# Kernel tuning notes

Measured on AMD Instinct MI355X. Metric: run time of the kernel, lower is better.

## Reference

```python
import jax, jax.numpy as jnp
import numpy as np

N_NODES = 10000
N_EDGES = 320000
D_IN = 256
D_HID = 256
N_TASKS = 128
N_GRAPHS = 128


def gcn_conv(x, W, b, src, dst, inv_sqrt_deg, n_nodes):
    # PyG GCNConv: x' = W x, then symmetric-normalized scatter-add over
    # edges (self-loops already included in src/dst), plus bias.
    h = x @ W  # [N, D_out]
    norm = inv_sqrt_deg[src] * inv_sqrt_deg[dst]  # [E+N]
    msg = h[src] * norm[:, None]  # [E+N, D_out] gathered messages
    out = jax.ops.segment_sum(msg, dst, num_segments=n_nodes)
    return out + b


def setup_inputs() -> dict:
    key = jax.random.key(0)
    ks = jax.random.split(key, 10)
    x = jax.random.normal(ks[0], (N_NODES, D_IN), dtype=jnp.float32)
    edge_index = jax.random.randint(ks[1], (2, N_EDGES), 0, N_NODES, dtype=jnp.int64)
    batch = jnp.sort(jax.random.randint(ks[2], (N_NODES,), 0, N_GRAPHS, dtype=jnp.int64))
    s = 1.0 / np.sqrt(D_HID)
    W1 = jax.random.uniform(ks[3], (D_IN, D_HID), jnp.float32, -s, s)
    b1 = jnp.zeros((D_HID,), jnp.float32)
    W2 = jax.random.uniform(ks[4], (D_HID, D_HID), jnp.float32, -s, s)
    b2 = jnp.zeros((D_HID,), jnp.float32)
    W3 = jax.random.uniform(ks[5], (D_HID, D_HID), jnp.float32, -s, s)
    b3 = jnp.zeros((D_HID,), jnp.float32)
    lin_w = jax.random.uniform(ks[6], (D_HID, N_TASKS), jnp.float32, -s, s)
    lin_b = jax.random.uniform(ks[7], (N_TASKS,), jnp.float32, -s, s)
    return {"x": x, "edge_index": edge_index, "batch": batch,
            "W1": W1, "b1": b1, "W2": W2, "b2": b2, "W3": W3, "b3": b3,
            "lin_w": lin_w, "lin_b": lin_b}


def reference(x, edge_index, batch, W1, b1, W2, b2, W3, b3, lin_w, lin_b):
    n = x.shape[0]
    loops = jnp.arange(n, dtype=edge_index.dtype)
    src = jnp.concatenate([edge_index[0], loops])  # add self-loops
    dst = jnp.concatenate([edge_index[1], loops])
    deg = jax.ops.segment_sum(jnp.ones_like(dst, dtype=x.dtype), dst, num_segments=n)
    inv_sqrt_deg = jnp.where(deg > 0, jax.lax.rsqrt(jnp.maximum(deg, 1.0)), 0.0)

    h = jax.nn.relu(gcn_conv(x, W1, b1, src, dst, inv_sqrt_deg, n))
    h = jax.nn.relu(gcn_conv(h, W2, b2, src, dst, inv_sqrt_deg, n))
    h = jax.nn.relu(gcn_conv(h, W3, b3, src, dst, inv_sqrt_deg, n))

    # global_mean_pool over graph ids
    sums = jax.ops.segment_sum(h, batch, num_segments=N_GRAPHS)  # [G, D]
    counts = jax.ops.segment_sum(jnp.ones((n,), h.dtype), batch, num_segments=N_GRAPHS)
    pooled = sums / jnp.maximum(counts, 1.0)[:, None]
    return pooled @ lin_w + lin_b  # [G, num_tasks]
```

## Files before the change

kernel.cpp:

```cpp
#include <hip/hip_runtime.h>

#define N_NODES  10000
#define N_EDGES  320000
#define D        256
#define N_TASKS  128
#define N_GRAPHS 128

#define CSR_BLOCKS 256
#define EPB (N_EDGES / CSR_BLOCKS)

typedef __attribute__((ext_vector_type(8))) _Float16 half8;
typedef __attribute__((ext_vector_type(4))) float floatx4;

__device__ __forceinline__ unsigned short f2h(float f) {
    _Float16 h = (_Float16)f;
    return *(unsigned short*)&h;
}
__device__ __forceinline__ float h2f(unsigned short u) {
    _Float16 h = *(_Float16*)&u;
    return (float)h;
}


__global__ __launch_bounds__(256) void histp_kernel(const int* __restrict__ dst,
                                                    unsigned short* __restrict__ histbuf,
                                                    unsigned short* __restrict__ rank) {
    __shared__ int h[N_NODES];
    int b = blockIdx.x, t = threadIdx.x;
    for (int i = t; i < N_NODES; i += 256) h[i] = 0;
    __syncthreads();
    int e0 = b * EPB;
    for (int i = t; i < EPB; i += 256) {
        int e = e0 + i;
        int r = atomicAdd(&h[dst[e]], 1);
        rank[e] = (unsigned short)r;
    }
    __syncthreads();
    unsigned short* outp = histbuf + (size_t)b * N_NODES;
    for (int i = t; i < N_NODES; i += 256) outp[i] = (unsigned short)h[i];
}

__global__ __launch_bounds__(256) void merge_kernel(unsigned short* __restrict__ histbuf,
                                                    int* __restrict__ cnt) {
    int n = blockIdx.x * 256 + threadIdx.x;
    if (n >= N_NODES) return;
    int run = 0;
#pragma unroll 1
    for (int b = 0; b < CSR_BLOCKS; b += 8) {
        int v0 = histbuf[(size_t)(b + 0) * N_NODES + n];
        int v1 = histbuf[(size_t)(b + 1) * N_NODES + n];
        int v2 = histbuf[(size_t)(b + 2) * N_NODES + n];
        int v3 = histbuf[(size_t)(b + 3) * N_NODES + n];
        int v4 = histbuf[(size_t)(b + 4) * N_NODES + n];
        int v5 = histbuf[(size_t)(b + 5) * N_NODES + n];
        int v6 = histbuf[(size_t)(b + 6) * N_NODES + n];
        int v7 = histbuf[(size_t)(b + 7) * N_NODES + n];
        histbuf[(size_t)(b + 0) * N_NODES + n] = (unsigned short)run; run += v0;
        histbuf[(size_t)(b + 1) * N_NODES + n] = (unsigned short)run; run += v1;
        histbuf[(size_t)(b + 2) * N_NODES + n] = (unsigned short)run; run += v2;
        histbuf[(size_t)(b + 3) * N_NODES + n] = (unsigned short)run; run += v3;
        histbuf[(size_t)(b + 4) * N_NODES + n] = (unsigned short)run; run += v4;
        histbuf[(size_t)(b + 5) * N_NODES + n] = (unsigned short)run; run += v5;
        histbuf[(size_t)(b + 6) * N_NODES + n] = (unsigned short)run; run += v6;
        histbuf[(size_t)(b + 7) * N_NODES + n] = (unsigned short)run; run += v7;
    }
    cnt[n] = run + 1;
}

__global__ __launch_bounds__(256) void scan_kernel(const int* __restrict__ cnt,
                                                   int* __restrict__ rowptr,
                                                   float* __restrict__ isd) {
    __shared__ int scnt[10240];
    __shared__ int part[256];
    const int CH = 40;
    int t = threadIdx.x;
    for (int i = t; i < 2500; i += 256) ((int4*)scnt)[i] = ((const int4*)cnt)[i];
    for (int i = 10000 + t; i < 10240; i += 256) scnt[i] = 1;
    __syncthreads();
    int base = t * CH;
    int s = 0;
#pragma unroll 8
    for (int i = 0; i < CH; ++i) s += scnt[base + i] - 1;
    part[t] = s;
    __syncthreads();
    for (int off = 1; off < 256; off <<= 1) {
        int v = (t >= off) ? part[t - off] : 0;
        __syncthreads();
        part[t] += v;
        __syncthreads();
    }
    int run = (t == 0) ? 0 : part[t - 1];
    for (int i = 0; i < CH; ++i) {
        int idx = base + i;
        if (idx < N_NODES) {
            rowptr[idx] = run;
            int c = scnt[idx];
            run += c - 1;
            isd[idx] = rsqrtf((float)c);
        }
    }
    if (t == 255) rowptr[N_NODES] = run;
}

__global__ __launch_bounds__(256) void scatter_kernel(const int* __restrict__ src,
                                                      const int* __restrict__ dst,
                                                      const unsigned short* __restrict__ rank,
                                                      const int* __restrict__ rowptr,
                                                      const unsigned short* __restrict__ histbuf,
                                                      const float* __restrict__ isd,
                                                      int2* __restrict__ edat) {
    int e = blockIdx.x * 256 + threadIdx.x;
    if (e >= N_EDGES) return;
    int b = e / EPB;
    int s = src[e], d = dst[e];
    int pos = rowptr[d] + (int)histbuf[(size_t)b * N_NODES + d] + (int)rank[e];
    edat[pos] = make_int2(s, __float_as_int(isd[s] * isd[d]));
}

__global__ __launch_bounds__(256) void wsplit_kernel(const float* __restrict__ W1,
                                                     const float* __restrict__ W2,
                                                     const float* __restrict__ W3,
                                                     unsigned short* __restrict__ wt) {
    __shared__ float t[32][33];
    int b = blockIdx.x;
    int w = b >> 6, tile = b & 63;
    int kt = (tile >> 3) << 5, nt = (tile & 7) << 5;
    const float* W = (w == 0) ? W1 : (w == 1) ? W2 : W3;
    int tid = threadIdx.x, r = tid >> 5, c = tid & 31;
#pragma unroll
    for (int i = 0; i < 4; ++i)
        t[r + 8 * i][c] = W[(size_t)(kt + r + 8 * i) * D + nt + c];
    __syncthreads();
    unsigned short* oh = wt + w * D * D;
#pragma unroll
    for (int i = 0; i < 4; ++i)
        oh[(size_t)(nt + r + 8 * i) * D + kt + c] = f2h(t[c][r + 8 * i]);
}

template <int F32IN>
__global__ __launch_bounds__(256) void mm_kernel(const void* __restrict__ Av,
                                                 const unsigned short* __restrict__ Wt,
                                                 unsigned short* __restrict__ C) {
    __shared__ unsigned short sA[64][40], sW[64][40];
    int tid = threadIdx.x;
    int lane = tid & 63, wid = tid >> 6;
    int wr = wid >> 1, wc = wid & 1;
    int row0 = blockIdx.x << 6;
    int n0 = blockIdx.y << 6;

    int sr = tid >> 2;
    int sk = (tid & 3) << 3;
    int arow = row0 + sr; if (arow >= N_NODES) arow = N_NODES - 1;
    const float*          pAf = (const float*)Av + (size_t)arow * D + sk;
    const unsigned short* pAh = (const unsigned short*)Av + (size_t)arow * D + sk;
    const unsigned short* pW  = Wt + (size_t)(n0 + sr) * D + sk;

    float4 rf0, rf1; uint4 rAh;
    if (F32IN) { rf0 = *(const float4*)pAf; rf1 = *(const float4*)(pAf + 4); }
    else       { rAh = *(const uint4*)pAh; }
    uint4 rW = *(const uint4*)pW;

    int fr = lane & 15;
    int fk = (lane >> 4) << 3;

    floatx4 acc00 = {0.f, 0.f, 0.f, 0.f};
    floatx4 acc01 = acc00, acc10 = acc00, acc11 = acc00;

#pragma unroll 1
    for (int step = 0; step < D / 32; ++step) {
        if (F32IN) {
            float vv[8] = {rf0.x, rf0.y, rf0.z, rf0.w, rf1.x, rf1.y, rf1.z, rf1.w};
            union { unsigned short u[8]; uint4 v; } ph;
#pragma unroll
            for (int j = 0; j < 8; ++j) ph.u[j] = f2h(vv[j]);
            *(uint4*)&sA[sr][sk] = ph.v;
        } else {
            *(uint4*)&sA[sr][sk] = rAh;
        }
        *(uint4*)&sW[sr][sk] = rW;
        __syncthreads();
        if (step < D / 32 - 1) {
            if (F32IN) {
                rf0 = *(const float4*)(pAf + (step + 1) * 32);
                rf1 = *(const float4*)(pAf + (step + 1) * 32 + 4);
            } else {
                rAh = *(const uint4*)(pAh + (step + 1) * 32);
            }
            rW = *(const uint4*)(pW + (step + 1) * 32);
        }
        half8 a0 = *(const half8*)&sA[(wr << 5) + fr][fk];
        half8 a1 = *(const half8*)&sA[(wr << 5) + 16 + fr][fk];
        half8 b0 = *(const half8*)&sW[(wc << 5) + fr][fk];
        half8 b1 = *(const half8*)&sW[(wc << 5) + 16 + fr][fk];
        acc00 = __builtin_amdgcn_mfma_f32_16x16x32_f16(a0, b0, acc00, 0, 0, 0);
        acc01 = __builtin_amdgcn_mfma_f32_16x16x32_f16(a0, b1, acc01, 0, 0, 0);
        acc10 = __builtin_amdgcn_mfma_f32_16x16x32_f16(a1, b0, acc10, 0, 0, 0);
        acc11 = __builtin_amdgcn_mfma_f32_16x16x32_f16(a1, b1, acc11, 0, 0, 0);
        __syncthreads();
    }

    int crow = (lane >> 4) << 2;
    int colbase = n0 + (wc << 5) + fr;
#pragma unroll
    for (int r = 0; r < 4; ++r) {
        int gr0 = row0 + (wr << 5) + crow + r;
        if (gr0 < N_NODES) {
            C[(size_t)gr0 * D + colbase]      = f2h(acc00[r]);
            C[(size_t)gr0 * D + colbase + 16] = f2h(acc01[r]);
        }
        int gr1 = gr0 + 16;
        if (gr1 < N_NODES) {
            C[(size_t)gr1 * D + colbase]      = f2h(acc10[r]);
            C[(size_t)gr1 * D + colbase + 16] = f2h(acc11[r]);
        }
    }
}

__device__ __forceinline__ void fma8(uint4 q, float wt, float* acc) {
    acc[0] = fmaf(h2f((unsigned short)(q.x & 0xffff)), wt, acc[0]);
    acc[1] = fmaf(h2f((unsigned short)(q.x >> 16)),    wt, acc[1]);
    acc[2] = fmaf(h2f((unsigned short)(q.y & 0xffff)), wt, acc[2]);
    acc[3] = fmaf(h2f((unsigned short)(q.y >> 16)),    wt, acc[3]);
    acc[4] = fmaf(h2f((unsigned short)(q.z & 0xffff)), wt, acc[4]);
    acc[5] = fmaf(h2f((unsigned short)(q.z >> 16)),    wt, acc[5]);
    acc[6] = fmaf(h2f((unsigned short)(q.w & 0xffff)), wt, acc[6]);
    acc[7] = fmaf(h2f((unsigned short)(q.w >> 16)),    wt, acc[7]);
}

__global__ __launch_bounds__(256) void agg_kernel(const unsigned short* __restrict__ h,
                                                  const int* __restrict__ rowptr,
                                                  const int2* __restrict__ edat,
                                                  const float* __restrict__ isd,
                                                  const float* __restrict__ bias,
                                                  unsigned short* __restrict__ outh) {
    int node = (blockIdx.x * blockDim.x + threadIdx.x) >> 6;
    if (node >= N_NODES) return;
    int lane = threadIdx.x & 63;
    int half = lane >> 5;
    int sub  = lane & 31;

    float acc[8] = {0.f, 0.f, 0.f, 0.f, 0.f, 0.f, 0.f, 0.f};

    float isd_i = isd[node];
    float selfw = half ? 0.f : isd_i * isd_i;
    uint4 qs = *(const uint4*)(h + (size_t)node * D + (sub << 3));
    fma8(qs, selfw, acc);

    int e0 = rowptr[node];
    int deg = rowptr[node + 1] - e0;
    for (int base = 0; base < deg; base += 64) {
        int n = deg - base; if (n > 64) n = 64;
        int2 ed = edat[e0 + base + ((lane < n) ? lane : 0)];
        int pairs = (n + 1) >> 1;
        for (int p0 = 0; p0 < pairs; p0 += 8) {
            uint4 q[8]; float wt[8];
#pragma unroll
            for (int u = 0; u < 8; ++u) {
                int idx = ((p0 + u) << 1) + half;
                int idc = (idx < n) ? idx : 0;
                int s = __shfl(ed.x, idc);
                wt[u] = (idx < n && (p0 + u) < pairs)
                            ? __int_as_float(__shfl(ed.y, idc)) : 0.f;
                q[u] = *(const uint4*)(h + (size_t)s * D + (sub << 3));
            }
#pragma unroll
            for (int u = 0; u < 8; ++u) fma8(q[u], wt[u], acc);
        }
    }

#pragma unroll
    for (int i = 0; i < 8; ++i) acc[i] += __shfl_xor(acc[i], 32);

    if (half == 0) {
        const float* bp = bias + (sub << 3);
        float4 b0 = *(const float4*)bp;
        float4 b1 = *(const float4*)(bp + 4);
        float r0 = fmaxf(acc[0] + b0.x, 0.f), r1 = fmaxf(acc[1] + b0.y, 0.f);
        float r2 = fmaxf(acc[2] + b0.z, 0.f), r3 = fmaxf(acc[3] + b0.w, 0.f);
        float r4 = fmaxf(acc[4] + b1.x, 0.f), r5 = fmaxf(acc[5] + b1.y, 0.f);
        float r6 = fmaxf(acc[6] + b1.z, 0.f), r7 = fmaxf(acc[7] + b1.w, 0.f);
        uint4 o;
        o.x = (unsigned)f2h(r0) | ((unsigned)f2h(r1) << 16);
        o.y = (unsigned)f2h(r2) | ((unsigned)f2h(r3) << 16);
        o.z = (unsigned)f2h(r4) | ((unsigned)f2h(r5) << 16);
        o.w = (unsigned)f2h(r6) | ((unsigned)f2h(r7) << 16);
        *(uint4*)(outh + (size_t)node * D + (sub << 3)) = o;
    }
}

__global__ __launch_bounds__(256) void poolfinal_kernel(const unsigned short* __restrict__ h,
                                                        const int* __restrict__ batch,
                                                        const float* __restrict__ lw,
                                                        const float* __restrict__ lb,
                                                        float* __restrict__ out) {
    __shared__ float part[4][D];
    __shared__ float p[D];
    int g = blockIdx.x;
    int tid = threadIdx.x, w = tid >> 6, lane = tid & 63;
    int lo = 0, hi = N_NODES;
    while (lo < hi) { int m = (lo + hi) >> 1; if (batch[m] < g) lo = m + 1; else hi = m; }
    int start = lo;
    hi = N_NODES;
    while (lo < hi) { int m = (lo + hi) >> 1; if (batch[m] <= g) lo = m + 1; else hi = m; }
    int end = lo;
    float4 acc = make_float4(0.f, 0.f, 0.f, 0.f);
    for (int nd = start + w; nd < end; nd += 4) {
        ushort4 q = reinterpret_cast<const ushort4*>(h + (size_t)nd * D)[lane];
        acc.x += h2f(q.x); acc.y += h2f(q.y); acc.z += h2f(q.z); acc.w += h2f(q.w);
    }
    reinterpret_cast<float4*>(part[w])[lane] = acc;
    __syncthreads();
    float invc = 1.f / (float)((end > start) ? (end - start) : 1);
    p[tid] = (part[0][tid] + part[1][tid] + part[2][tid] + part[3][tid]) * invc;
    __syncthreads();
    if (tid < N_TASKS) {
        float a = lb[tid];
        for (int k = 0; k < D; ++k) a = fmaf(p[k], lw[k * N_TASKS + tid], a);
        out[g * N_TASKS + tid] = a;
    }
}

extern "C" void kernel_launch(void* const* d_in, const int* in_sizes, int n_in,
                              void* d_out, int out_size, void* d_ws, size_t ws_size,
                              hipStream_t stream) {
    const float* x   = (const float*)d_in[0];
    const int*   ei  = (const int*)d_in[1];
    const int*   bat = (const int*)d_in[2];
    const float* W1  = (const float*)d_in[3];
    const float* b1  = (const float*)d_in[4];
    const float* W2  = (const float*)d_in[5];
    const float* b2  = (const float*)d_in[6];
    const float* W3  = (const float*)d_in[7];
    const float* b3  = (const float*)d_in[8];
    const float* lw  = (const float*)d_in[9];
    const float* lb  = (const float*)d_in[10];
    float* out = (float*)d_out;

    const int* src = ei;
    const int* dst = ei + N_EDGES;

    char* ws = (char*)d_ws;
    unsigned short* gH      = (unsigned short*)(ws + 0);
    unsigned short* hH      = (unsigned short*)(ws + 5120000);
    unsigned short* Wt      = (unsigned short*)(ws + 10240000);
    float*          isd     = (float*)         (ws + 10633216);
    int*            cnt     = (int*)           (ws + 10673216);
    int*            rowptr  = (int*)           (ws + 10713216);
    int2*           edat    = (int2*)          (ws + 10753232);
    unsigned short* histbuf = (unsigned short*)(ws + 13313232);
    unsigned short* rank    = (unsigned short*)(ws + 18433232);

    histp_kernel<<<CSR_BLOCKS, 256, 0, stream>>>(dst, histbuf, rank);
    merge_kernel<<<(N_NODES + 255) / 256, 256, 0, stream>>>(histbuf, cnt);
    scan_kernel<<<1, 256, 0, stream>>>(cnt, rowptr, isd);
    scatter_kernel<<<(N_EDGES + 255) / 256, 256, 0, stream>>>(src, dst, rank, rowptr,
                                                              histbuf, isd, edat);
    wsplit_kernel<<<3 * 64, 256, 0, stream>>>(W1, W2, W3, Wt);

    dim3 mmgrid((N_NODES + 63) / 64, D / 64);
    const int AGG_BLOCKS = N_NODES / 4;

    mm_kernel<1><<<mmgrid, 256, 0, stream>>>(x, Wt, hH);
    agg_kernel<<<AGG_BLOCKS, 256, 0, stream>>>(hH, rowptr, edat, isd, b1, gH);
    mm_kernel<0><<<mmgrid, 256, 0, stream>>>(gH, Wt + D * D, hH);
    agg_kernel<<<AGG_BLOCKS, 256, 0, stream>>>(hH, rowptr, edat, isd, b2, gH);
    mm_kernel<0><<<mmgrid, 256, 0, stream>>>(gH, Wt + 2 * D * D, hH);
    agg_kernel<<<AGG_BLOCKS, 256, 0, stream>>>(hH, rowptr, edat, isd, b3, gH);

    poolfinal_kernel<<<N_GRAPHS, 256, 0, stream>>>(gH, bat, lw, lb, out);
}
```

Baseline: 144.3 us.

## Cut CSR histogram blocks, pack histogram stores, use two 128-wide K stages in GEMM

The CSR build now uses 64 histogram blocks instead of 256, so the merge pass reads a quarter of the partial histograms, and each block writes its counts as packed 32-bit pairs. The GEMM kernel replaces eight 32-wide K steps with two 128-wide stages held in larger shared tiles, which cuts the barrier count and issues more global loads per thread at once. The trade-offs are fewer, longer histogram blocks with more atomic contention each, and more shared memory and registers per GEMM block, which may lower occupancy. The rank buffer offset moves down to match the smaller histogram buffer.

```diff
diff --git a/kernel.cpp b/kernel.cpp
--- a/kernel.cpp
+++ b/kernel.cpp
@@ -6,7 +6,7 @@
 #define N_TASKS  128
 #define N_GRAPHS 128
 
-#define CSR_BLOCKS 256
+#define CSR_BLOCKS 64
 #define EPB (N_EDGES / CSR_BLOCKS)
 
 typedef __attribute__((ext_vector_type(8))) _Float16 half8;
@@ -36,8 +36,9 @@
         rank[e] = (unsigned short)r;
     }
     __syncthreads();
-    unsigned short* outp = histbuf + (size_t)b * N_NODES;
-    for (int i = t; i < N_NODES; i += 256) outp[i] = (unsigned short)h[i];
+    int* outp = (int*)(histbuf + (size_t)b * N_NODES);
+    for (int i = t; i < N_NODES / 2; i += 256)
+        outp[i] = (h[2 * i] & 0xffff) | (h[2 * i + 1] << 16);
 }
 
 __global__ __launch_bounds__(256) void merge_kernel(unsigned short* __restrict__ histbuf,
@@ -141,62 +142,95 @@
 __global__ __launch_bounds__(256) void mm_kernel(const void* __restrict__ Av,
                                                  const unsigned short* __restrict__ Wt,
                                                  unsigned short* __restrict__ C) {
-    __shared__ unsigned short sA[64][40], sW[64][40];
+    __shared__ unsigned short sA[64][136], sW[64][136];
     int tid = threadIdx.x;
     int lane = tid & 63, wid = tid >> 6;
     int wr = wid >> 1, wc = wid & 1;
     int row0 = blockIdx.x << 6;
     int n0 = blockIdx.y << 6;
 
-    int sr = tid >> 2;
-    int sk = (tid & 3) << 3;
-    int arow = row0 + sr; if (arow >= N_NODES) arow = N_NODES - 1;
-    const float*          pAf = (const float*)Av + (size_t)arow * D + sk;
-    const unsigned short* pAh = (const unsigned short*)Av + (size_t)arow * D + sk;
-    const unsigned short* pW  = Wt + (size_t)(n0 + sr) * D + sk;
-
-    float4 rf0, rf1; uint4 rAh;
-    if (F32IN) { rf0 = *(const float4*)pAf; rf1 = *(const float4*)(pAf + 4); }
-    else       { rAh = *(const uint4*)pAh; }
-    uint4 rW = *(const uint4*)pW;
+    const unsigned short* pA16 = (const unsigned short*)Av;
+    const float*          pA32 = (const float*)Av;
+
+    int lr = tid >> 2;
+    int lc = tid & 3;
+    int arow = row0 + lr; if (arow >= N_NODES) arow = N_NODES - 1;
+
+    uint4 ra[4], rw[4];
+#pragma unroll
+    for (int j = 0; j < 4; ++j) {
+        int c16 = lc + 4 * j;
+        if (F32IN) {
+            float4 f0 = *(const float4*)(pA32 + (size_t)arow * D + c16 * 8);
+            float4 f1 = *(const float4*)(pA32 + (size_t)arow * D + c16 * 8 + 4);
+            union { unsigned short u[8]; uint4 v; } p;
+            p.u[0] = f2h(f0.x); p.u[1] = f2h(f0.y); p.u[2] = f2h(f0.z); p.u[3] = f2h(f0.w);
+            p.u[4] = f2h(f1.x); p.u[5] = f2h(f1.y); p.u[6] = f2h(f1.z); p.u[7] = f2h(f1.w);
+            ra[j] = p.v;
+        } else {
+            ra[j] = *(const uint4*)(pA16 + (size_t)arow * D + c16 * 8);
+        }
+        rw[j] = *(const uint4*)(Wt + (size_t)(n0 + lr) * D + c16 * 8);
+    }
+#pragma unroll
+    for (int j = 0; j < 4; ++j) {
+        int c16 = lc + 4 * j;
+        *(uint4*)&sA[lr][c16 * 8] = ra[j];
+        *(uint4*)&sW[lr][c16 * 8] = rw[j];
+    }
+    __syncthreads();
+
+#pragma unroll
+    for (int j = 0; j < 4; ++j) {
+        int c16 = lc + 4 * j;
+        if (F32IN) {
+            float4 f0 = *(const float4*)(pA32 + (size_t)arow * D + 128 + c16 * 8);
+            float4 f1 = *(const float4*)(pA32 + (size_t)arow * D + 128 + c16 * 8 + 4);
+            union { unsigned short u[8]; uint4 v; } p;
+            p.u[0] = f2h(f0.x); p.u[1] = f2h(f0.y); p.u[2] = f2h(f0.z); p.u[3] = f2h(f0.w);
+            p.u[4] = f2h(f1.x); p.u[5] = f2h(f1.y); p.u[6] = f2h(f1.z); p.u[7] = f2h(f1.w);
+            ra[j] = p.v;
+        } else {
+            ra[j] = *(const uint4*)(pA16 + (size_t)arow * D + 128 + c16 * 8);
+        }
+        rw[j] = *(const uint4*)(Wt + (size_t)(n0 + lr) * D + 128 + c16 * 8);
+    }
 
     int fr = lane & 15;
     int fk = (lane >> 4) << 3;
-
     floatx4 acc00 = {0.f, 0.f, 0.f, 0.f};
     floatx4 acc01 = acc00, acc10 = acc00, acc11 = acc00;
 
-#pragma unroll 1
-    for (int step = 0; step < D / 32; ++step) {
-        if (F32IN) {
-            float vv[8] = {rf0.x, rf0.y, rf0.z, rf0.w, rf1.x, rf1.y, rf1.z, rf1.w};
-            union { unsigned short u[8]; uint4 v; } ph;
-#pragma unroll
-            for (int j = 0; j < 8; ++j) ph.u[j] = f2h(vv[j]);
-            *(uint4*)&sA[sr][sk] = ph.v;
-        } else {
-            *(uint4*)&sA[sr][sk] = rAh;
-        }
-        *(uint4*)&sW[sr][sk] = rW;
-        __syncthreads();
-        if (step < D / 32 - 1) {
-            if (F32IN) {
-                rf0 = *(const float4*)(pAf + (step + 1) * 32);
-                rf1 = *(const float4*)(pAf + (step + 1) * 32 + 4);
-            } else {
-                rAh = *(const uint4*)(pAh + (step + 1) * 32);
-            }
-            rW = *(const uint4*)(pW + (step + 1) * 32);
-        }
-        half8 a0 = *(const half8*)&sA[(wr << 5) + fr][fk];
-        half8 a1 = *(const half8*)&sA[(wr << 5) + 16 + fr][fk];
-        half8 b0 = *(const half8*)&sW[(wc << 5) + fr][fk];
-        half8 b1 = *(const half8*)&sW[(wc << 5) + 16 + fr][fk];
+#pragma unroll
+    for (int ks = 0; ks < 4; ++ks) {
+        half8 a0 = *(const half8*)&sA[(wr << 5) + fr][fk + ks * 32];
+        half8 a1 = *(const half8*)&sA[(wr << 5) + 16 + fr][fk + ks * 32];
+        half8 b0 = *(const half8*)&sW[(wc << 5) + fr][fk + ks * 32];
+        half8 b1 = *(const half8*)&sW[(wc << 5) + 16 + fr][fk + ks * 32];
         acc00 = __builtin_amdgcn_mfma_f32_16x16x32_f16(a0, b0, acc00, 0, 0, 0);
         acc01 = __builtin_amdgcn_mfma_f32_16x16x32_f16(a0, b1, acc01, 0, 0, 0);
         acc10 = __builtin_amdgcn_mfma_f32_16x16x32_f16(a1, b0, acc10, 0, 0, 0);
         acc11 = __builtin_amdgcn_mfma_f32_16x16x32_f16(a1, b1, acc11, 0, 0, 0);
-        __syncthreads();
+    }
+    __syncthreads();
+
+#pragma unroll
+    for (int j = 0; j < 4; ++j) {
+        int c16 = lc + 4 * j;
+        *(uint4*)&sA[lr][c16 * 8] = ra[j];
+        *(uint4*)&sW[lr][c16 * 8] = rw[j];
+    }
+    __syncthreads();
+#pragma unroll
+    for (int ks = 0; ks < 4; ++ks) {
+        half8 a0 = *(const half8*)&sA[(wr << 5) + fr][fk + ks * 32];
+        half8 a1 = *(const half8*)&sA[(wr << 5) + 16 + fr][fk + ks * 32];
+        half8 b0 = *(const half8*)&sW[(wc << 5) + fr][fk + ks * 32];
+        half8 b1 = *(const half8*)&sW[(wc << 5) + 16 + fr][fk + ks * 32];
+        acc00 = __builtin_amdgcn_mfma_f32_16x16x32_f16(a0, b0, acc00, 0, 0, 0);
+        acc01 = __builtin_amdgcn_mfma_f32_16x16x32_f16(a0, b1, acc01, 0, 0, 0);
+        acc10 = __builtin_amdgcn_mfma_f32_16x16x32_f16(a1, b0, acc10, 0, 0, 0);
+        acc11 = __builtin_amdgcn_mfma_f32_16x16x32_f16(a1, b1, acc11, 0, 0, 0);
     }
 
     int crow = (lane >> 4) << 2;
@@ -348,7 +382,7 @@
     int*            rowptr  = (int*)           (ws + 10713216);
     int2*           edat    = (int2*)          (ws + 10753232);
     unsigned short* histbuf = (unsigned short*)(ws + 13313232);
-    unsigned short* rank    = (unsigned short*)(ws + 18433232);
+    unsigned short* rank    = (unsigned short*)(ws + 14593232);
 
     histp_kernel<<<CSR_BLOCKS, 256, 0, stream>>>(dst, histbuf, rank);
     merge_kernel<<<(N_NODES + 255) / 256, 256, 0, stream>>>(histbuf, cnt);
```

After: 157.7 us. 1.09x slower.

## Merge independent prep kernels into combined launches to cut launch count

Applied to the files above, without the earlier changes.

Folds the weight transpose/convert work into the histogram kernel as extra blocks, and fuses the edge scatter with the first-layer matmul into one heterogeneous launch. Histogram output is written as packed 32-bit pairs instead of 16-bit stores. This removes two kernel launches and their serialization gaps, and lets independent work overlap. In exchange, the histogram blocks' large LDS allocation is also reserved by the weight-split blocks, and the mixed matmul/scatter launch has uneven block costs.

```diff
diff --git a/kernel.cpp b/kernel.cpp
--- a/kernel.cpp
+++ b/kernel.cpp
@@ -8,6 +8,9 @@
 
 #define CSR_BLOCKS 256
 #define EPB (N_EDGES / CSR_BLOCKS)
+#define MM_BX 157
+#define MM_BLOCKS (MM_BX * 4)
+#define SCAT_BLOCKS ((N_EDGES + 255) / 256)
 
 typedef __attribute__((ext_vector_type(8))) _Float16 half8;
 typedef __attribute__((ext_vector_type(4))) float floatx4;
@@ -22,23 +25,47 @@
 }
 
 
-__global__ __launch_bounds__(256) void histp_kernel(const int* __restrict__ dst,
-                                                    unsigned short* __restrict__ histbuf,
-                                                    unsigned short* __restrict__ rank) {
+__global__ __launch_bounds__(256) void prep_kernel(const int* __restrict__ dst,
+                                                   unsigned short* __restrict__ histbuf,
+                                                   unsigned short* __restrict__ rank,
+                                                   const float* __restrict__ W1,
+                                                   const float* __restrict__ W2,
+                                                   const float* __restrict__ W3,
+                                                   unsigned short* __restrict__ wt) {
     __shared__ int h[N_NODES];
-    int b = blockIdx.x, t = threadIdx.x;
-    for (int i = t; i < N_NODES; i += 256) h[i] = 0;
-    __syncthreads();
-    int e0 = b * EPB;
-    for (int i = t; i < EPB; i += 256) {
-        int e = e0 + i;
-        int r = atomicAdd(&h[dst[e]], 1);
-        rank[e] = (unsigned short)r;
-    }
-    __syncthreads();
-    unsigned short* outp = histbuf + (size_t)b * N_NODES;
-    for (int i = t; i < N_NODES; i += 256) outp[i] = (unsigned short)h[i];
-}
+    __shared__ float t[32][33];
+    int t0 = threadIdx.x;
+    if (blockIdx.x < CSR_BLOCKS) {
+        int b = blockIdx.x;
+        for (int i = t0; i < N_NODES; i += 256) h[i] = 0;
+        __syncthreads();
+        int e0 = b * EPB;
+        for (int i = t0; i < EPB; i += 256) {
+            int e = e0 + i;
+            int r = atomicAdd(&h[dst[e]], 1);
+            rank[e] = (unsigned short)r;
+        }
+        __syncthreads();
+        int* outp = (int*)(histbuf + (size_t)b * N_NODES);
+        for (int i = t0; i < N_NODES / 2; i += 256)
+            outp[i] = (h[2 * i] & 0xffff) | (h[2 * i + 1] << 16);
+    } else {
+        int b = blockIdx.x - CSR_BLOCKS;
+        int w = b >> 6, tile = b & 63;
+        int kt = (tile >> 3) << 5, nt = (tile & 7) << 5;
+        const float* W = (w == 0) ? W1 : (w == 1) ? W2 : W3;
+        int r = t0 >> 5, c = t0 & 31;
+#pragma unroll
+        for (int i = 0; i < 4; ++i)
+            t[r + 8 * i][c] = W[(size_t)(kt + r + 8 * i) * D + nt + c];
+        __syncthreads();
+        unsigned short* oh = wt + w * D * D;
+#pragma unroll
+        for (int i = 0; i < 4; ++i)
+            oh[(size_t)(nt + r + 8 * i) * D + kt + c] = f2h(t[c][r + 8 * i]);
+    }
+}
+
 
 __global__ __launch_bounds__(256) void merge_kernel(unsigned short* __restrict__ histbuf,
                                                     int* __restrict__ cnt) {
@@ -67,6 +94,7 @@
     cnt[n] = run + 1;
 }
 
+
 __global__ __launch_bounds__(256) void scan_kernel(const int* __restrict__ cnt,
                                                    int* __restrict__ rowptr,
                                                    float* __restrict__ isd) {
@@ -102,51 +130,15 @@
     if (t == 255) rowptr[N_NODES] = run;
 }
 
-__global__ __launch_bounds__(256) void scatter_kernel(const int* __restrict__ src,
-                                                      const int* __restrict__ dst,
-                                                      const unsigned short* __restrict__ rank,
-                                                      const int* __restrict__ rowptr,
-                                                      const unsigned short* __restrict__ histbuf,
-                                                      const float* __restrict__ isd,
-                                                      int2* __restrict__ edat) {
-    int e = blockIdx.x * 256 + threadIdx.x;
-    if (e >= N_EDGES) return;
-    int b = e / EPB;
-    int s = src[e], d = dst[e];
-    int pos = rowptr[d] + (int)histbuf[(size_t)b * N_NODES + d] + (int)rank[e];
-    edat[pos] = make_int2(s, __float_as_int(isd[s] * isd[d]));
-}
-
-__global__ __launch_bounds__(256) void wsplit_kernel(const float* __restrict__ W1,
-                                                     const float* __restrict__ W2,
-                                                     const float* __restrict__ W3,
-                                                     unsigned short* __restrict__ wt) {
-    __shared__ float t[32][33];
-    int b = blockIdx.x;
-    int w = b >> 6, tile = b & 63;
-    int kt = (tile >> 3) << 5, nt = (tile & 7) << 5;
-    const float* W = (w == 0) ? W1 : (w == 1) ? W2 : W3;
-    int tid = threadIdx.x, r = tid >> 5, c = tid & 31;
-#pragma unroll
-    for (int i = 0; i < 4; ++i)
-        t[r + 8 * i][c] = W[(size_t)(kt + r + 8 * i) * D + nt + c];
-    __syncthreads();
-    unsigned short* oh = wt + w * D * D;
-#pragma unroll
-    for (int i = 0; i < 4; ++i)
-        oh[(size_t)(nt + r + 8 * i) * D + kt + c] = f2h(t[c][r + 8 * i]);
-}
 
 template <int F32IN>
-__global__ __launch_bounds__(256) void mm_kernel(const void* __restrict__ Av,
-                                                 const unsigned short* __restrict__ Wt,
-                                                 unsigned short* __restrict__ C) {
-    __shared__ unsigned short sA[64][40], sW[64][40];
-    int tid = threadIdx.x;
+__device__ __forceinline__ void mm_body(unsigned short (*sA)[40], unsigned short (*sW)[40],
+                                        const void* __restrict__ Av,
+                                        const unsigned short* __restrict__ Wt,
+                                        unsigned short* __restrict__ C,
+                                        int row0, int n0, int tid) {
     int lane = tid & 63, wid = tid >> 6;
     int wr = wid >> 1, wc = wid & 1;
-    int row0 = blockIdx.x << 6;
-    int n0 = blockIdx.y << 6;
 
     int sr = tid >> 2;
     int sk = (tid & 3) << 3;
@@ -212,6 +204,40 @@
         if (gr1 < N_NODES) {
             C[(size_t)gr1 * D + colbase]      = f2h(acc10[r]);
             C[(size_t)gr1 * D + colbase + 16] = f2h(acc11[r]);
+        }
+    }
+}
+
+template <int F32IN>
+__global__ __launch_bounds__(256) void mm_kernel(const void* __restrict__ Av,
+                                                 const unsigned short* __restrict__ Wt,
+                                                 unsigned short* __restrict__ C) {
+    __shared__ unsigned short sA[64][40], sW[64][40];
+    mm_body<F32IN>(sA, sW, Av, Wt, C, blockIdx.x << 6, blockIdx.y << 6, threadIdx.x);
+}
+
+__global__ __launch_bounds__(256) void scatmm_kernel(const float* __restrict__ x,
+                                                     const unsigned short* __restrict__ Wt,
+                                                     unsigned short* __restrict__ C,
+                                                     const int* __restrict__ src,
+                                                     const int* __restrict__ dst,
+                                                     const unsigned short* __restrict__ rank,
+                                                     const int* __restrict__ rowptr,
+                                                     const unsigned short* __restrict__ histbuf,
+                                                     const float* __restrict__ isd,
+                                                     int2* __restrict__ edat) {
+    __shared__ unsigned short sA[64][40], sW[64][40];
+    if (blockIdx.x < MM_BLOCKS) {
+        int row0 = (blockIdx.x % MM_BX) << 6;
+        int n0   = (blockIdx.x / MM_BX) << 6;
+        mm_body<1>(sA, sW, x, Wt, C, row0, n0, threadIdx.x);
+    } else {
+        int e = (blockIdx.x - MM_BLOCKS) * 256 + threadIdx.x;
+        if (e < N_EDGES) {
+            int b = e / EPB;
+            int s = src[e], d = dst[e];
+            int pos = rowptr[d] + (int)histbuf[(size_t)b * N_NODES + d] + (int)rank[e];
+            edat[pos] = make_int2(s, __float_as_int(isd[s] * isd[d]));
         }
     }
 }
@@ -350,22 +376,19 @@
     unsigned short* histbuf = (unsigned short*)(ws + 13313232);
     unsigned short* rank    = (unsigned short*)(ws + 18433232);
 
-    histp_kernel<<<CSR_BLOCKS, 256, 0, stream>>>(dst, histbuf, rank);
+    prep_kernel<<<CSR_BLOCKS + 192, 256, 0, stream>>>(dst, histbuf, rank, W1, W2, W3, Wt);
     merge_kernel<<<(N_NODES + 255) / 256, 256, 0, stream>>>(histbuf, cnt);
     scan_kernel<<<1, 256, 0, stream>>>(cnt, rowptr, isd);
-    scatter_kernel<<<(N_EDGES + 255) / 256, 256, 0, stream>>>(src, dst, rank, rowptr,
-                                                              histbuf, isd, edat);
-    wsplit_kernel<<<3 * 64, 256, 0, stream>>>(W1, W2, W3, Wt);
-
-    dim3 mmgrid((N_NODES + 63) / 64, D / 64);
+    scatmm_kernel<<<MM_BLOCKS + SCAT_BLOCKS, 256, 0, stream>>>(x, Wt, hH, src, dst, rank,
+                                                               rowptr, histbuf, isd, edat);
+
+    dim3 mmgrid(MM_BX, D / 64);
     const int AGG_BLOCKS = N_NODES / 4;
 
-    mm_kernel<1><<<mmgrid, 256, 0, stream>>>(x, Wt, hH);
     agg_kernel<<<AGG_BLOCKS, 256, 0, stream>>>(hH, rowptr, edat, isd, b1, gH);
     mm_kernel<0><<<mmgrid, 256, 0, stream>>>(gH, Wt + D * D, hH);
     agg_kernel<<<AGG_BLOCKS, 256, 0, stream>>>(hH, rowptr, edat, isd, b2, gH);
     mm_kernel<0><<<mmgrid, 256, 0, stream>>>(gH, Wt + 2 * D * D, hH);
     agg_kernel<<<AGG_BLOCKS, 256, 0, stream>>>(hH, rowptr, edat, isd, b3, gH);
-
     poolfinal_kernel<<<N_GRAPHS, 256, 0, stream>>>(gH, bat, lw, lb, out);
 }
```

After: 139.6 us. 1.03x faster.
